# Optimization experiments

Measured on AMD Instinct MI355X. Metric: run time of the kernel, lower is better.

Reference implementation:

```python
import jax, jax.numpy as jnp
import numpy as np
import math

LN_EPS = 1e-5

def _ln(x, g, b):
    m = jnp.mean(x, -1, keepdims=True)
    v = jnp.mean((x - m) ** 2, -1, keepdims=True)
    return (x - m) / jnp.sqrt(v + LN_EPS) * g + b

def setup_inputs() -> dict:
    key = jax.random.key(0)
    ks = jax.random.split(key, 16)
    B, N, D, V = 2, 512, 128, 16
    w = lambda k, shape: jax.random.normal(k, shape, jnp.float32) * 0.02
    return {
        "scalar": jax.random.normal(ks[0], (B, N, D), jnp.float32),
        "vector": jax.random.normal(ks[1], (B, N, 3, V), jnp.float32),
        "coords": jax.random.normal(ks[2], (B, N, 3), jnp.float32),
        "w_q": w(ks[3], (D, D)), "b_q": jnp.zeros((D,), jnp.float32),
        "w_k": w(ks[4], (D, D)), "b_k": jnp.zeros((D,), jnp.float32),
        "w_v": w(ks[5], (D, D)), "b_v": jnp.zeros((D,), jnp.float32),
        "w_d1": w(ks[6], (1, D)), "b_d1": jnp.zeros((D,), jnp.float32),
        "w_d2": w(ks[7], (D, D)), "b_d2": jnp.zeros((D,), jnp.float32),
        "w_g": w(ks[8], (D, V)), "b_g": jnp.zeros((V,), jnp.float32),
        "w_o": w(ks[9], (D, D)), "b_o": jnp.zeros((D,), jnp.float32),
        "w_f1": w(ks[10], (D, 2 * D)), "b_f1": jnp.zeros((2 * D,), jnp.float32),
        "w_f2": w(ks[11], (2 * D, D)), "b_f2": jnp.zeros((D,), jnp.float32),
        "w_vo": w(ks[12], (V, V)), "b_vo": jnp.zeros((V,), jnp.float32),
        "g_s": jnp.ones((D,), jnp.float32), "be_s": jnp.zeros((D,), jnp.float32),
        "g_v": jnp.ones((V,), jnp.float32), "be_v": jnp.zeros((V,), jnp.float32),
    }

def reference(scalar, vector, coords, w_q, b_q, w_k, b_k, w_v, b_v,
              w_d1, b_d1, w_d2, b_d2, w_g, b_g, w_o, b_o,
              w_f1, b_f1, w_f2, b_f2, w_vo, b_vo, g_s, be_s, g_v, be_v):
    D = scalar.shape[-1]
    # pairwise geometry: [B,N,N,3], [B,N,N,1]
    rel = coords[:, :, None, :] - coords[:, None, :, :]
    dist = jnp.linalg.norm(rel, axis=-1, keepdims=True)
    direction = rel / jnp.maximum(dist, 1e-6)
    sn = _ln(scalar, g_s, be_s)
    q = sn @ w_q + b_q
    k = sn @ w_k + b_k
    v = sn @ w_v + b_v
    # distance-conditioned bias: [B,N,N,D]
    bias = jax.nn.gelu(dist @ w_d1 + b_d1, approximate=False) @ w_d2 + b_d2
    # q_i . (k_j + bias_ij) / sqrt(D)
    logits = (jnp.einsum('bid,bjd->bij', q, k)
              + jnp.einsum('bid,bijd->bij', q, bias)) / math.sqrt(D)
    attn = jax.nn.softmax(logits, axis=-1)
    # sum_j attn_ij * (v_j + bias_ij)
    upd = jnp.einsum('bij,bjd->bid', attn, v) + jnp.einsum('bij,bijd->bid', attn, bias)
    scalar = scalar + (upd @ w_o + b_o)
    h = _ln(scalar, g_s, be_s)
    scalar = scalar + (jax.nn.gelu(h @ w_f1 + b_f1, approximate=False) @ w_f2 + b_f2)
    gate = jax.nn.sigmoid(scalar @ w_g + b_g)  # [B,N,V]
    # sum_j attn_ij * (vector_j + dir_ij * gate_i) decomposed (same math, no BxNxNx3xV tensor)
    agg = (jnp.einsum('bij,bjcv->bicv', attn, vector)
           + jnp.einsum('bij,bijc->bic', attn, direction)[..., None] * gate[:, :, None, :])
    projected = _ln(agg, g_v, be_v) @ w_vo + b_vo
    return scalar, vector + projected
```

## Files before the change

### kernel.cpp

```cpp
#include <hip/hip_runtime.h>
#include <math.h>

#define D 128
#define F 256
#define V 16
#define NSEQ 512
#define NROW 1024
#define MQ 7

__device__ __forceinline__ float gelu_exact(float x) {
    return 0.5f * x * (1.0f + erff(x * 0.70710678118654752f));
}

__device__ __forceinline__ float waveSum(float v) {
#pragma unroll
    for (int o = 32; o; o >>= 1) v += __shfl_xor(v, o);
    return v;
}
__device__ __forceinline__ float waveMax(float v) {
#pragma unroll
    for (int o = 32; o; o >>= 1) v = fmaxf(v, __shfl_xor(v, o));
    return v;
}

__device__ __forceinline__ void build_A(const float* __restrict__ w_d1,
                                        const float* __restrict__ b_d1,
                                        float* A_s, int t) {
    if (t < D) {
        const float gam[MQ] = {0.f, 0.5f, 0.39894228f, 0.f, -0.06649038f, 0.f,
                               0.0099735570f};
        float w = w_d1[t], b = b_d1[t];
        float wp[MQ], bp[MQ];
        wp[0] = 1.f; bp[0] = 1.f;
#pragma unroll
        for (int i = 1; i < MQ; i++) { wp[i] = wp[i - 1] * w; bp[i] = bp[i - 1] * b; }
        float A[MQ];
#pragma unroll
        for (int m = 0; m < MQ; m++) A[m] = 0.f;
#pragma unroll
        for (int k = 1; k < MQ; k++) {
            float g = gam[k];
            if (g == 0.f) continue;
            float C = 1.f;
            for (int m = 0; m <= k; m++) {
                A[m] = fmaf(g * C, wp[m] * bp[k - m], A[m]);
                C = C * (float)(k - m) / (float)(m + 1);
            }
        }
#pragma unroll
        for (int m = 0; m < MQ; m++) A_s[t * MQ + m] = A[m];
    }
}

__global__ __launch_bounds__(1024, 8) void k1_qkv(
    const float* __restrict__ scalar,
    const float* __restrict__ w_q, const float* __restrict__ b_q,
    const float* __restrict__ w_k, const float* __restrict__ b_k,
    const float* __restrict__ w_v, const float* __restrict__ b_v,
    const float* __restrict__ w_d1, const float* __restrict__ b_d1,
    const float* __restrict__ w_d2,
    const float* __restrict__ g_s, const float* __restrict__ be_s,
    float* __restrict__ qg, float* __restrict__ kTg, float* __restrict__ vg,
    float* __restrict__ Gg)
{
    const int t = threadIdx.x, wvid = t >> 6, ln = t & 63;
    const int r0 = blockIdx.x * 4;
    const int l = t & 127, rr = (t >> 7) & 3;
    __shared__ __align__(16) float snT[D][4];
    __shared__ float k_s[4][D];
    __shared__ __align__(16) float P3[3][8][4][D];
    __shared__ float A_sG[D * MQ];
    __shared__ float redA[16], redB[16];

    float x = scalar[(size_t)(r0 + rr) * D + l];
    { float s = waveSum(x); if (ln == 0) redA[wvid] = s; }
    __syncthreads();
    float mean = (redA[2 * rr] + redA[2 * rr + 1]) * (1.0f / 128.0f);
    float dv = x - mean;
    { float s = waveSum(dv * dv); if (ln == 0) redB[wvid] = s; }
    __syncthreads();
    float var = (redB[2 * rr] + redB[2 * rr + 1]) * (1.0f / 128.0f);
    if (t < 512) snT[l][rr] = dv * rsqrtf(var + 1e-5f) * g_s[l] + be_s[l];
    __syncthreads();

    if (t < 768) {
        const int g = t >> 7;
        const int mat = (g < 3) ? g : g - 3, eh = (g < 3) ? 0 : 1;
        const int es = (t >> 5) & 3, lq = t & 31, l0 = lq * 4;
        const int e0 = eh * 64 + es * 16;
        const float* W = (mat == 0) ? w_q : (mat == 1) ? w_k : w_v;
        float acc[4][4];
#pragma unroll
        for (int r2 = 0; r2 < 4; r2++)
#pragma unroll
            for (int c2 = 0; c2 < 4; c2++) acc[r2][c2] = 0.f;
#pragma unroll 4
        for (int e = e0; e < e0 + 16; e++) {
            float4 w4 = *(const float4*)&W[e * D + l0];
            float4 s4 = *(const float4*)&snT[e][0];
            const float sr[4] = {s4.x, s4.y, s4.z, s4.w};
#pragma unroll
            for (int r2 = 0; r2 < 4; r2++) {
                acc[r2][0] = fmaf(sr[r2], w4.x, acc[r2][0]);
                acc[r2][1] = fmaf(sr[r2], w4.y, acc[r2][1]);
                acc[r2][2] = fmaf(sr[r2], w4.z, acc[r2][2]);
                acc[r2][3] = fmaf(sr[r2], w4.w, acc[r2][3]);
            }
        }
        const int pi = eh * 4 + es;
#pragma unroll
        for (int r2 = 0; r2 < 4; r2++)
            *(float4*)&P3[mat][pi][r2][l0] =
                make_float4(acc[r2][0], acc[r2][1], acc[r2][2], acc[r2][3]);
    }
    __syncthreads();

#pragma unroll
    for (int pass = 0; pass < 2; pass++) {
        const int o = t + pass * 1024;
        if (o < 1536) {
            const int mat = o >> 9, row = (o >> 7) & 3, l2 = o & 127;
            float acc = 0.f;
#pragma unroll
            for (int eo = 0; eo < 8; eo++) acc += P3[mat][eo][row][l2];
            if (mat == 0)      qg[(size_t)(r0 + row) * D + l2] = acc + b_q[l2];
            else if (mat == 1) k_s[row][l2] = acc + b_k[l2];
            else               vg[(size_t)(r0 + row) * D + l2] = acc + b_v[l2];
        }
    }
    __syncthreads();

    if (t < 128) {
        float4 kv = make_float4(k_s[0][t], k_s[1][t], k_s[2][t], k_s[3][t]);
        *(float4*)&kTg[(size_t)t * NROW + r0] = kv;
    }

    if (blockIdx.x < MQ) {
        build_A(w_d1, b_d1, A_sG, t);
        __syncthreads();
        const int m = blockIdx.x;
        if (t < D) {
            float acc = 0.f;
#pragma unroll 4
            for (int e = 0; e < D; e++)
                acc = fmaf(w_d2[e * D + t], A_sG[e * MQ + m], acc);
            Gg[t * MQ + m] = acc;
        }
    }
}

__global__ __launch_bounds__(1024, 4) void k23(
    const float* __restrict__ coords, const float* __restrict__ vecin,
    const float* __restrict__ scalar,
    const float* __restrict__ qg, const float* __restrict__ kTg,
    const float* __restrict__ vg, const float* __restrict__ Gg,
    const float* __restrict__ b_d2,
    const float* __restrict__ w_o, const float* __restrict__ b_o,
    const float* __restrict__ w_f1, const float* __restrict__ b_f1,
    const float* __restrict__ w_f2, const float* __restrict__ b_f2,
    const float* __restrict__ w_g, const float* __restrict__ b_g,
    const float* __restrict__ w_vo, const float* __restrict__ b_vo,
    const float* __restrict__ g_s, const float* __restrict__ be_s,
    const float* __restrict__ g_v, const float* __restrict__ be_v,
    float* __restrict__ out_s, float* __restrict__ out_v)
{
    const int t = threadIdx.x, wvid = t >> 6, ln = t & 63;
    const int r0 = blockIdx.x * 4, b = blockIdx.x >> 7;
    __shared__ __align__(16) float AT[NSEQ * 4];
    __shared__ __align__(16) float PB[16384];
    __shared__ __align__(16) float qT[D][4];
    __shared__ float Gl[D * MQ];
    __shared__ float P_s[4][MQ];
    __shared__ __align__(16) float updT[D][4], hT[D][4], s1T[D][4];
    __shared__ __align__(16) float t2T[F][4];
    __shared__ float S_s[4][MQ], adir_s[4][3], avec_s[4][48];
    __shared__ float redA[16], redB[16];
    __shared__ float wredM[16][10];
    __shared__ float gate_s[4][V], lnv_s[4][48];
    __shared__ __align__(16) float avp[16][4][48];

    float vpre[32];
    if (ln < 48) {
        const float* vp = vecin + ((size_t)b * NSEQ + 32 * wvid) * 48 + ln;
#pragma unroll
        for (int jj = 0; jj < 32; jj++) vpre[jj] = vp[(size_t)jj * 48];
    }

    if (t < 512) qT[t & 127][t >> 7] = qg[(size_t)(r0 + (t >> 7)) * D + (t & 127)];
    if (t < D * MQ) Gl[t] = Gg[t];
    __syncthreads();

    {
        const int dd = t & 127, row = (t >> 7) & 3;
        float qv = qT[dd][row];
        float pa[MQ];
#pragma unroll
        for (int m = 0; m < MQ; m++) pa[m] = qv * Gl[dd * MQ + m];
        pa[0] = fmaf(qv, b_d2[dd], pa[0]);
#pragma unroll
        for (int m = 0; m < MQ; m++) {
            float s = waveSum(pa[m]);
            if (ln == 0) wredM[wvid][m] = s;
        }
    }
    __syncthreads();
    if (t < 4 * MQ) {
        const int hh = t / MQ, m = t % MQ;
        P_s[hh][m] = (wredM[hh * 2][m] + wredM[hh * 2 + 1][m]
                    + wredM[8 + hh * 2][m] + wredM[8 + hh * 2 + 1][m]) * 0.5f;
    }

    {
        const int jq = t & 127, j0 = jq * 4, eq = t >> 7, e0 = eq * 16;
        const float* ke = kTg + (size_t)e0 * NROW + (size_t)b * NSEQ + j0;
        float acc[4][4];
#pragma unroll
        for (int i = 0; i < 4; i++)
#pragma unroll
            for (int k2 = 0; k2 < 4; k2++) acc[i][k2] = 0.f;
#pragma unroll 4
        for (int e = 0; e < 16; e++) {
            float4 kv = *(const float4*)&ke[(size_t)e * NROW];
            float4 q4 = *(const float4*)&qT[e0 + e][0];
            const float qr[4] = {q4.x, q4.y, q4.z, q4.w};
#pragma unroll
            for (int rr2 = 0; rr2 < 4; rr2++) {
                acc[rr2][0] = fmaf(qr[rr2], kv.x, acc[rr2][0]);
                acc[rr2][1] = fmaf(qr[rr2], kv.y, acc[rr2][1]);
                acc[rr2][2] = fmaf(qr[rr2], kv.z, acc[rr2][2]);
                acc[rr2][3] = fmaf(qr[rr2], kv.w, acc[rr2][3]);
            }
        }
#pragma unroll
        for (int rr2 = 0; rr2 < 4; rr2++)
            *(float4*)&PB[(eq * 4 + rr2) * 512 + j0] =
                make_float4(acc[rr2][0], acc[rr2][1], acc[rr2][2], acc[rr2][3]);
    }
    __syncthreads();

    const int row = t >> 8, jh = t & 255;
    const int rA = r0 + row;
    const float cix = coords[(size_t)rA * 3 + 0];
    const float ciy = coords[(size_t)rA * 3 + 1];
    const float ciz = coords[(size_t)rA * 3 + 2];
    const float* cj0 = coords + ((size_t)b * NSEQ + jh) * 3;
    const float* cj1 = cj0 + 256 * 3;
    float rx0 = cix - cj0[0], ry0 = ciy - cj0[1], rz0 = ciz - cj0[2];
    float rx1 = cix - cj1[0], ry1 = ciy - cj1[1], rz1 = ciz - cj1[2];
    float dj0 = sqrtf(rx0 * rx0 + ry0 * ry0 + rz0 * rz0);
    float dj1 = sqrtf(rx1 * rx1 + ry1 * ry1 + rz1 * rz1);
    float qk0 = 0.f, qk1 = 0.f;
#pragma unroll
    for (int eq = 0; eq < 8; eq++) {
        qk0 += PB[(eq * 4 + row) * 512 + jh];
        qk1 += PB[(eq * 4 + row) * 512 + jh + 256];
    }
    float bias0 = P_s[row][MQ - 1], bias1 = bias0;
#pragma unroll
    for (int m = MQ - 2; m >= 0; m--) {
        bias0 = fmaf(bias0, dj0, P_s[row][m]);
        bias1 = fmaf(bias1, dj1, P_s[row][m]);
    }
    const float sc = 0.08838834764831844f;
    float lg0 = (qk0 + bias0) * sc;
    float lg1 = (qk1 + bias1) * sc;

    { float mx = waveMax(fmaxf(lg0, lg1)); if (ln == 0) redA[wvid] = mx; }
    __syncthreads();
    float mx = fmaxf(fmaxf(redA[4 * row], redA[4 * row + 1]),
                     fmaxf(redA[4 * row + 2], redA[4 * row + 3]));
    float p0 = __expf(lg0 - mx), p1 = __expf(lg1 - mx);
    { float s = waveSum(p0 + p1); if (ln == 0) redB[wvid] = s; }
    __syncthreads();
    float ls = redB[4 * row] + redB[4 * row + 1]
             + redB[4 * row + 2] + redB[4 * row + 3];
    float inv = 1.0f / ls;
    float a0 = p0 * inv, a1 = p1 * inv;
    AT[jh * 4 + row] = a0;
    AT[(jh + 256) * 4 + row] = a1;

    {
        float red[10];
        float w0 = a0, w1 = a1;
#pragma unroll
        for (int m = 0; m < MQ; m++) { red[m] = w0 + w1; w0 *= dj0; w1 *= dj1; }
        float ia0 = a0 * __builtin_amdgcn_rcpf(fmaxf(dj0, 1e-6f));
        float ia1 = a1 * __builtin_amdgcn_rcpf(fmaxf(dj1, 1e-6f));
        red[7] = ia0 * rx0 + ia1 * rx1;
        red[8] = ia0 * ry0 + ia1 * ry1;
        red[9] = ia0 * rz0 + ia1 * rz1;
#pragma unroll
        for (int m = 0; m < 10; m++) {
            float s = waveSum(red[m]);
            if (ln == 0) wredM[wvid][m] = s;
        }
    }
    __syncthreads();
    if (t < 40) {
        const int hh = t / 10, m = t % 10;
        float s = wredM[4 * hh][m] + wredM[4 * hh + 1][m]
                + wredM[4 * hh + 2][m] + wredM[4 * hh + 3][m];
        if (m < MQ) S_s[hh][m] = s;
        else        adir_s[hh][m - MQ] = s;
    }

    {
        const int dq = t & 31, d0 = dq * 4, jo = t >> 5, jb = 16 * jo;
        const float* vb = vg + ((size_t)b * NSEQ + jb) * D + d0;
        float acc[4][4];
#pragma unroll
        for (int i = 0; i < 4; i++)
#pragma unroll
            for (int k2 = 0; k2 < 4; k2++) acc[i][k2] = 0.f;
#pragma unroll 4
        for (int jj = 0; jj < 16; jj++) {
            float4 at = *(const float4*)&AT[(jb + jj) * 4];
            float4 vv = *(const float4*)&vb[(size_t)jj * D];
            const float ar[4] = {at.x, at.y, at.z, at.w};
#pragma unroll
            for (int rr2 = 0; rr2 < 4; rr2++) {
                acc[rr2][0] = fmaf(ar[rr2], vv.x, acc[rr2][0]);
                acc[rr2][1] = fmaf(ar[rr2], vv.y, acc[rr2][1]);
                acc[rr2][2] = fmaf(ar[rr2], vv.z, acc[rr2][2]);
                acc[rr2][3] = fmaf(ar[rr2], vv.w, acc[rr2][3]);
            }
        }
#pragma unroll
        for (int rr2 = 0; rr2 < 4; rr2++)
            *(float4*)&PB[(jo * 4 + rr2) * 128 + d0] =
                make_float4(acc[rr2][0], acc[rr2][1], acc[rr2][2], acc[rr2][3]);
    }
    if (ln < 48) {
        const int jb = 32 * wvid;
        float c[4] = {0.f, 0.f, 0.f, 0.f};
#pragma unroll
        for (int jj = 0; jj < 32; jj++) {
            float4 at = *(const float4*)&AT[(jb + jj) * 4];
            c[0] = fmaf(at.x, vpre[jj], c[0]);
            c[1] = fmaf(at.y, vpre[jj], c[1]);
            c[2] = fmaf(at.z, vpre[jj], c[2]);
            c[3] = fmaf(at.w, vpre[jj], c[3]);
        }
#pragma unroll
        for (int rr2 = 0; rr2 < 4; rr2++) avp[wvid][rr2][ln] = c[rr2];
    }
    __syncthreads();

    if (t < 512) {
        const int rw = t >> 7, l = t & 127;
        float acc = 0.f;
#pragma unroll
        for (int jo = 0; jo < 32; jo++) acc += PB[(jo * 4 + rw) * 128 + l];
        float aa = 0.f;
#pragma unroll
        for (int m = 0; m < MQ; m++) aa = fmaf(Gl[l * MQ + m], S_s[rw][m], aa);
        updT[l][rw] = acc + aa + b_d2[l];
    } else if (t - 512 < 192) {
        const int idx = t - 512, rw = idx / 48, i2 = idx % 48;
        float s = 0.f;
#pragma unroll
        for (int w2 = 0; w2 < 16; w2++) s += avp[w2][rw][i2];
        avec_s[rw][i2] = s;
    }
    __syncthreads();

    {
        const int eo = t >> 7, l = t & 127, e0 = 16 * eo;
        float c[4] = {0.f, 0.f, 0.f, 0.f};
#pragma unroll 4
        for (int e = e0; e < e0 + 16; e++) {
            float4 up = *(const float4*)&updT[e][0];
            float wv = w_o[e * D + l];
            c[0] = fmaf(up.x, wv, c[0]); c[1] = fmaf(up.y, wv, c[1]);
            c[2] = fmaf(up.z, wv, c[2]); c[3] = fmaf(up.w, wv, c[3]);
        }
#pragma unroll
        for (int rr2 = 0; rr2 < 4; rr2++) PB[(eo * 4 + rr2) * 128 + l] = c[rr2];
    }
    __syncthreads();
    float xln = 0.f;
    {
        const int rw = (t >> 7) & 3, l = t & 127;
        if (t < 512) {
            float acc = 0.f;
#pragma unroll
            for (int eo = 0; eo < 8; eo++) acc += PB[(eo * 4 + rw) * 128 + l];
            xln = scalar[(size_t)(r0 + rw) * D + l] + acc + b_o[l];
            s1T[l][rw] = xln;
        }
        float s = waveSum(xln);
        if (t < 512 && ln == 0) redA[wvid] = s;
    }
    __syncthreads();
    float dvv = 0.f;
    if (t < 512) {
        const int rw = (t >> 7) & 3;
        float mean = (redA[2 * rw] + redA[2 * rw + 1]) * (1.0f / 128.0f);
        dvv = xln - mean;
    }
    {
        float s = waveSum(dvv * dvv);
        if (t < 512 && ln == 0) redB[wvid] = s;
    }
    __syncthreads();
    if (t < 512) {
        const int rw = (t >> 7) & 3, l = t & 127;
        float var = (redB[2 * rw] + redB[2 * rw + 1]) * (1.0f / 128.0f);
        hT[l][rw] = dvv * rsqrtf(var + 1e-5f) * g_s[l] + be_s[l];
    }
    __syncthreads();

    {
        const int f = t & 255, eq = t >> 8, e0 = 32 * eq;
        float c[4] = {0.f, 0.f, 0.f, 0.f};
#pragma unroll 4
        for (int e = e0; e < e0 + 32; e++) {
            float4 hv = *(const float4*)&hT[e][0];
            float wv = w_f1[e * F + f];
            c[0] = fmaf(hv.x, wv, c[0]); c[1] = fmaf(hv.y, wv, c[1]);
            c[2] = fmaf(hv.z, wv, c[2]); c[3] = fmaf(hv.w, wv, c[3]);
        }
#pragma unroll
        for (int rr2 = 0; rr2 < 4; rr2++) PB[(eq * 4 + rr2) * 256 + f] = c[rr2];
    }
    __syncthreads();
    {
        const int rw = t >> 8, f = t & 255;
        float acc = 0.f;
#pragma unroll
        for (int eq = 0; eq < 4; eq++) acc += PB[(eq * 4 + rw) * 256 + f];
        t2T[f][rw] = gelu_exact(acc + b_f1[f]);
    }
    __syncthreads();

    {
        const int fo = t >> 7, l = t & 127, f0 = 32 * fo;
        float c[4] = {0.f, 0.f, 0.f, 0.f};
#pragma unroll 4
        for (int f = f0; f < f0 + 32; f++) {
            float4 tv = *(const float4*)&t2T[f][0];
            float wv = w_f2[f * D + l];
            c[0] = fmaf(tv.x, wv, c[0]); c[1] = fmaf(tv.y, wv, c[1]);
            c[2] = fmaf(tv.z, wv, c[2]); c[3] = fmaf(tv.w, wv, c[3]);
        }
#pragma unroll
        for (int rr2 = 0; rr2 < 4; rr2++) PB[(fo * 4 + rr2) * 128 + l] = c[rr2];
    }
    __syncthreads();
    if (t < 512) {
        const int rw = t >> 7, l = t & 127;
        float acc = 0.f;
#pragma unroll
        for (int fo = 0; fo < 8; fo++) acc += PB[(fo * 4 + rw) * 128 + l];
        float v2 = s1T[l][rw] + acc + b_f2[l];
        out_s[(size_t)(r0 + rw) * D + l] = v2;
        s1T[l][rw] = v2;
    }
    __syncthreads();

    if (t < 256) {
        const int rw = wvid, vv = ln & 15, dh = ln >> 4, d0 = dh * 32;
        float aa = 0.f;
#pragma unroll 4
        for (int dd = d0; dd < d0 + 32; dd++)
            aa = fmaf(s1T[dd][rw], w_g[dd * V + vv], aa);
        aa += __shfl_xor(aa, 16);
        aa += __shfl_xor(aa, 32);
        if (dh == 0)
            gate_s[rw][vv] = 1.0f / (1.0f + __expf(-(aa + b_g[vv])));
    }
    __syncthreads();

    if (t < 192) {
        const int rw = t / 48, idx = t % 48, c = idx >> 4, vv = idx & 15;
        float agg = avec_s[rw][idx] + adir_s[rw][c] * gate_s[rw][vv];
        float s = agg;
#pragma unroll
        for (int o = 8; o; o >>= 1) s += __shfl_xor(s, o, 16);
        float mean = s * (1.0f / 16.0f);
        float e = agg - mean;
        float s2 = e * e;
#pragma unroll
        for (int o = 8; o; o >>= 1) s2 += __shfl_xor(s2, o, 16);
        float rstd = rsqrtf(s2 * (1.0f / 16.0f) + 1e-5f);
        lnv_s[rw][idx] = e * rstd * g_v[vv] + be_v[vv];
    }
    __syncthreads();
    if (t < 192) {
        const int rw = t / 48, idx = t % 48, c = idx >> 4, vv = idx & 15;
        const int rwg = r0 + rw;
        float aa = b_vo[vv];
#pragma unroll
        for (int w2 = 0; w2 < V; w2++)
            aa = fmaf(lnv_s[rw][c * V + w2], w_vo[w2 * V + vv], aa);
        out_v[(size_t)rwg * 48 + idx] = vecin[(size_t)rwg * 48 + idx] + aa;
    }
}

extern "C" void kernel_launch(void* const* d_in, const int* in_sizes, int n_in,
                              void* d_out, int out_size, void* d_ws, size_t ws_size,
                              hipStream_t stream)
{
    (void)in_sizes; (void)n_in; (void)out_size; (void)ws_size;
    const float* scalar = (const float*)d_in[0];
    const float* vecin  = (const float*)d_in[1];
    const float* coords = (const float*)d_in[2];
    const float* w_q  = (const float*)d_in[3];  const float* b_q  = (const float*)d_in[4];
    const float* w_k  = (const float*)d_in[5];  const float* b_k  = (const float*)d_in[6];
    const float* w_v  = (const float*)d_in[7];  const float* b_v  = (const float*)d_in[8];
    const float* w_d1 = (const float*)d_in[9];  const float* b_d1 = (const float*)d_in[10];
    const float* w_d2 = (const float*)d_in[11]; const float* b_d2 = (const float*)d_in[12];
    const float* w_g  = (const float*)d_in[13]; const float* b_g  = (const float*)d_in[14];
    const float* w_o  = (const float*)d_in[15]; const float* b_o  = (const float*)d_in[16];
    const float* w_f1 = (const float*)d_in[17]; const float* b_f1 = (const float*)d_in[18];
    const float* w_f2 = (const float*)d_in[19]; const float* b_f2 = (const float*)d_in[20];
    const float* w_vo = (const float*)d_in[21]; const float* b_vo = (const float*)d_in[22];
    const float* g_s  = (const float*)d_in[23]; const float* be_s = (const float*)d_in[24];
    const float* g_v  = (const float*)d_in[25]; const float* be_v = (const float*)d_in[26];

    float* ws  = (float*)d_ws;
    float* qg  = ws;
    float* kTg = ws + 131072;
    float* vg  = ws + 262144;
    float* Gg  = ws + 393216;

    float* out_s = (float*)d_out;
    float* out_v = out_s + 131072;

    hipLaunchKernelGGL(k1_qkv, dim3(NROW / 4), dim3(1024), 0, stream,
                       scalar, w_q, b_q, w_k, b_k, w_v, b_v, w_d1, b_d1,
                       w_d2, g_s, be_s, qg, kTg, vg, Gg);
    hipLaunchKernelGGL(k23, dim3(NROW / 4), dim3(1024), 0, stream,
                       coords, vecin, scalar, qg, kTg, vg, Gg,
                       b_d2, w_o, b_o, w_f1, b_f1, w_f2, b_f2,
                       w_g, b_g, w_vo, b_vo, g_s, be_s, g_v, be_v,
                       out_s, out_v);
}
```

Measured before the change: 150.7 us.

## Halve shared partial buffer and register tiles to raise k23 occupancy

```diff
diff --git a/kernel.cpp b/kernel.cpp
--- a/kernel.cpp
+++ b/kernel.cpp
@@ -149,7 +149,7 @@
     }
 }
 
-__global__ __launch_bounds__(1024, 4) void k23(
+__global__ __launch_bounds__(1024, 8) void k23(
     const float* __restrict__ coords, const float* __restrict__ vecin,
     const float* __restrict__ scalar,
     const float* __restrict__ qg, const float* __restrict__ kTg,
@@ -167,7 +167,7 @@
     const int t = threadIdx.x, wvid = t >> 6, ln = t & 63;
     const int r0 = blockIdx.x * 4, b = blockIdx.x >> 7;
     __shared__ __align__(16) float AT[NSEQ * 4];
-    __shared__ __align__(16) float PB[16384];
+    __shared__ __align__(16) float PB[8192];
     __shared__ __align__(16) float qT[D][4];
     __shared__ float Gl[D * MQ];
     __shared__ float P_s[4][MQ];
@@ -179,13 +179,6 @@
     __shared__ float gate_s[4][V], lnv_s[4][48];
     __shared__ __align__(16) float avp[16][4][48];
 
-    float vpre[32];
-    if (ln < 48) {
-        const float* vp = vecin + ((size_t)b * NSEQ + 32 * wvid) * 48 + ln;
-#pragma unroll
-        for (int jj = 0; jj < 32; jj++) vpre[jj] = vp[(size_t)jj * 48];
-    }
-
     if (t < 512) qT[t & 127][t >> 7] = qg[(size_t)(r0 + (t >> 7)) * D + (t & 127)];
     if (t < D * MQ) Gl[t] = Gg[t];
     __syncthreads();
@@ -211,30 +204,25 @@
     }
 
     {
-        const int jq = t & 127, j0 = jq * 4, eq = t >> 7, e0 = eq * 16;
+        const int jq = t & 255, j0 = jq * 2, eq = t >> 8, e0 = eq * 32;
         const float* ke = kTg + (size_t)e0 * NROW + (size_t)b * NSEQ + j0;
-        float acc[4][4];
-#pragma unroll
-        for (int i = 0; i < 4; i++)
-#pragma unroll
-            for (int k2 = 0; k2 < 4; k2++) acc[i][k2] = 0.f;
-#pragma unroll 4
-        for (int e = 0; e < 16; e++) {
-            float4 kv = *(const float4*)&ke[(size_t)e * NROW];
+        float c0[4], c1[4];
+#pragma unroll
+        for (int i = 0; i < 4; i++) { c0[i] = 0.f; c1[i] = 0.f; }
+#pragma unroll 8
+        for (int e = 0; e < 32; e++) {
+            float2 kv = *(const float2*)&ke[(size_t)e * NROW];
             float4 q4 = *(const float4*)&qT[e0 + e][0];
             const float qr[4] = {q4.x, q4.y, q4.z, q4.w};
 #pragma unroll
             for (int rr2 = 0; rr2 < 4; rr2++) {
-                acc[rr2][0] = fmaf(qr[rr2], kv.x, acc[rr2][0]);
-                acc[rr2][1] = fmaf(qr[rr2], kv.y, acc[rr2][1]);
-                acc[rr2][2] = fmaf(qr[rr2], kv.z, acc[rr2][2]);
-                acc[rr2][3] = fmaf(qr[rr2], kv.w, acc[rr2][3]);
+                c0[rr2] = fmaf(qr[rr2], kv.x, c0[rr2]);
+                c1[rr2] = fmaf(qr[rr2], kv.y, c1[rr2]);
             }
         }
 #pragma unroll
         for (int rr2 = 0; rr2 < 4; rr2++)
-            *(float4*)&PB[(eq * 4 + rr2) * 512 + j0] =
-                make_float4(acc[rr2][0], acc[rr2][1], acc[rr2][2], acc[rr2][3]);
+            *(float2*)&PB[(eq * 4 + rr2) * 512 + j0] = make_float2(c0[rr2], c1[rr2]);
     }
     __syncthreads();
 
@@ -251,7 +239,7 @@
     float dj1 = sqrtf(rx1 * rx1 + ry1 * ry1 + rz1 * rz1);
     float qk0 = 0.f, qk1 = 0.f;
 #pragma unroll
-    for (int eq = 0; eq < 8; eq++) {
+    for (int eq = 0; eq < 4; eq++) {
         qk0 += PB[(eq * 4 + row) * 512 + jh];
         qk1 += PB[(eq * 4 + row) * 512 + jh + 256];
     }
@@ -305,41 +293,38 @@
     }
 
     {
-        const int dq = t & 31, d0 = dq * 4, jo = t >> 5, jb = 16 * jo;
+        const int dq = t & 63, d0 = dq * 2, jo = t >> 6, jb = 32 * jo;
         const float* vb = vg + ((size_t)b * NSEQ + jb) * D + d0;
-        float acc[4][4];
-#pragma unroll
-        for (int i = 0; i < 4; i++)
-#pragma unroll
-            for (int k2 = 0; k2 < 4; k2++) acc[i][k2] = 0.f;
-#pragma unroll 4
-        for (int jj = 0; jj < 16; jj++) {
+        float c0[4], c1[4];
+#pragma unroll
+        for (int i = 0; i < 4; i++) { c0[i] = 0.f; c1[i] = 0.f; }
+#pragma unroll 8
+        for (int jj = 0; jj < 32; jj++) {
             float4 at = *(const float4*)&AT[(jb + jj) * 4];
-            float4 vv = *(const float4*)&vb[(size_t)jj * D];
+            float2 vv = *(const float2*)&vb[(size_t)jj * D];
             const float ar[4] = {at.x, at.y, at.z, at.w};
 #pragma unroll
             for (int rr2 = 0; rr2 < 4; rr2++) {
-                acc[rr2][0] = fmaf(ar[rr2], vv.x, acc[rr2][0]);
-                acc[rr2][1] = fmaf(ar[rr2], vv.y, acc[rr2][1]);
-                acc[rr2][2] = fmaf(ar[rr2], vv.z, acc[rr2][2]);
-                acc[rr2][3] = fmaf(ar[rr2], vv.w, acc[rr2][3]);
+                c0[rr2] = fmaf(ar[rr2], vv.x, c0[rr2]);
+                c1[rr2] = fmaf(ar[rr2], vv.y, c1[rr2]);
             }
         }
 #pragma unroll
         for (int rr2 = 0; rr2 < 4; rr2++)
-            *(float4*)&PB[(jo * 4 + rr2) * 128 + d0] =
-                make_float4(acc[rr2][0], acc[rr2][1], acc[rr2][2], acc[rr2][3]);
+            *(float2*)&PB[(jo * 4 + rr2) * 128 + d0] = make_float2(c0[rr2], c1[rr2]);
     }
     if (ln < 48) {
         const int jb = 32 * wvid;
+        const float* vp = vecin + ((size_t)b * NSEQ + jb) * 48 + ln;
         float c[4] = {0.f, 0.f, 0.f, 0.f};
-#pragma unroll
+#pragma unroll 4
         for (int jj = 0; jj < 32; jj++) {
             float4 at = *(const float4*)&AT[(jb + jj) * 4];
-            c[0] = fmaf(at.x, vpre[jj], c[0]);
-            c[1] = fmaf(at.y, vpre[jj], c[1]);
-            c[2] = fmaf(at.z, vpre[jj], c[2]);
-            c[3] = fmaf(at.w, vpre[jj], c[3]);
+            float vv = vp[(size_t)jj * 48];
+            c[0] = fmaf(at.x, vv, c[0]);
+            c[1] = fmaf(at.y, vv, c[1]);
+            c[2] = fmaf(at.z, vv, c[2]);
+            c[3] = fmaf(at.w, vv, c[3]);
         }
 #pragma unroll
         for (int rr2 = 0; rr2 < 4; rr2++) avp[wvid][rr2][ln] = c[rr2];
@@ -350,7 +335,7 @@
         const int rw = t >> 7, l = t & 127;
         float acc = 0.f;
 #pragma unroll
-        for (int jo = 0; jo < 32; jo++) acc += PB[(jo * 4 + rw) * 128 + l];
+        for (int jo = 0; jo < 16; jo++) acc += PB[(jo * 4 + rw) * 128 + l];
         float aa = 0.f;
 #pragma unroll
         for (int m = 0; m < MQ; m++) aa = fmaf(Gl[l * MQ + m], S_s[rw][m], aa);
```

Result: slower. 164.3 us (+9.0%).
